# Kernel tuning notes

Measured on AMD Instinct MI355X. Metric: run time of the kernel, lower is better.

The kernel has to match this reference:

```python
import jax, jax.numpy as jnp
import numpy as np

N_NODES = 100000
N_EDGES = 3200000
NFEAT = 256
HDIM = 64
NCLASS = 64
K = 4
ALPHA = 0.1


def setup_inputs() -> dict:
    key = jax.random.key(0)
    k1, k2, k3, k4, k5, k6 = jax.random.split(key, 6)
    x = jax.random.normal(k1, (N_NODES, NFEAT), dtype=jnp.float32)
    edge_index = jax.random.randint(k2, (2, N_EDGES), 0, N_NODES, dtype=jnp.int64)
    W_in = jax.random.normal(k3, (HDIM, NFEAT), dtype=jnp.float32) * (1.0 / np.sqrt(NFEAT))
    b_in = jax.random.normal(k4, (HDIM,), dtype=jnp.float32) * 0.01
    W_out = jax.random.normal(k5, (NCLASS, HDIM), dtype=jnp.float32) * (1.0 / np.sqrt(HDIM))
    b_out = jax.random.normal(k6, (NCLASS,), dtype=jnp.float32) * 0.01
    return {"x": x, "edge_index": edge_index, "W_in": W_in, "b_in": b_in,
            "W_out": W_out, "b_out": b_out}


def _gcn_norm(edge_index, n_nodes):
    # add self-loops, then symmetric normalization (PyG gcn_norm defaults)
    loops = jnp.arange(n_nodes, dtype=edge_index.dtype)
    src = jnp.concatenate([edge_index[0], loops])
    dst = jnp.concatenate([edge_index[1], loops])
    deg = jax.ops.segment_sum(jnp.ones_like(dst, dtype=jnp.float32), dst,
                              num_segments=n_nodes)
    dinv = jnp.where(deg > 0, 1.0 / jnp.sqrt(deg), 0.0)
    w = dinv[src] * dinv[dst]  # [E+N]
    return src, dst, w


def reference(x, edge_index, W_in, b_in, W_out, b_out):
    n = x.shape[0]
    src, dst, w = _gcn_norm(edge_index, n)
    h = x @ W_in.T + b_in                      # [N, 64]
    x0 = h
    for _ in range(K):                         # APPNP: (1-a) * A_hat h + a * x0
        agg = jax.ops.segment_sum(w[:, None] * h[src], dst, num_segments=n)
        h = (1.0 - ALPHA) * agg + ALPHA * x0
    h = jax.nn.relu(h)
    return h @ W_out.T + b_out                 # [N, nclass]
```

## Files before the change

### kernel.cpp

```cpp
#include <hip/hip_runtime.h>
#include <hip/hip_fp16.h>

#define NN 100000
#define NE 3200000
#define NFEAT 256
#define HDIM 64
#define NCLASS 64
#define ALPHA 0.1f
#define CAP 80

#define NB 256
#define BKN 391
#define EBLK (NE / 256)
#define BCAP 24
#define RCAP 96

typedef _Float16 half8 __attribute__((ext_vector_type(8)));
typedef float f32x4 __attribute__((ext_vector_type(4)));


__device__ inline unsigned pack4_fp8(float a, float b, float c, float d) {
    unsigned v = 0;
    v = __builtin_amdgcn_cvt_pk_fp8_f32(a, b, v, false);
    v = __builtin_amdgcn_cvt_pk_fp8_f32(c, d, v, true);
    return v;
}

__device__ inline void acc8_fp8(uint2 r, float m, float* acc) {
    auto l0 = __builtin_amdgcn_cvt_pk_f32_fp8(r.x, false);
    auto h0 = __builtin_amdgcn_cvt_pk_f32_fp8(r.x, true);
    auto l1 = __builtin_amdgcn_cvt_pk_f32_fp8(r.y, false);
    auto h1 = __builtin_amdgcn_cvt_pk_f32_fp8(r.y, true);
    acc[0] = fmaf(m, l0[0], acc[0]); acc[1] = fmaf(m, l0[1], acc[1]);
    acc[2] = fmaf(m, h0[0], acc[2]); acc[3] = fmaf(m, h0[1], acc[3]);
    acc[4] = fmaf(m, l1[0], acc[4]); acc[5] = fmaf(m, l1[1], acc[5]);
    acc[6] = fmaf(m, h1[0], acc[6]); acc[7] = fmaf(m, h1[1], acc[7]);
}


__global__ __launch_bounds__(1024) void bucket_edges(const int* __restrict__ ei,
                                                     unsigned* __restrict__ pairs,
                                                     int* __restrict__ cntg) {
    __shared__ unsigned buf[NB][BCAP];
    __shared__ int cnt[NB];
    __shared__ int rcur[NB];
    int blk = blockIdx.x;
    int t = threadIdx.x;
    int e0 = blk * EBLK;
    for (int i = t; i < NB; i += 1024) { cnt[i] = 0; rcur[i] = 0; }
    __syncthreads();

    for (int eb = 0; eb < EBLK; eb += 1024) {
        bool act = (eb + t) < EBLK;
        if (act) {
            int e = e0 + eb + t;
            unsigned d = (unsigned)ei[NE + e];
            unsigned src = (unsigned)ei[e];
            unsigned b = d / BKN;
            unsigned w = (src << 9) | (d - b * BKN);
            int p = atomicAdd(&cnt[b], 1);
            if (p < BCAP) buf[b][p] = w;
        }
        __syncthreads();
        int lane = t & 63, wv = t >> 6;
        for (int j = 0; j < 16; j++) {
            int b2 = wv * 16 + j;
            int c = cnt[b2]; if (c > BCAP) c = BCAP;
            int rb = rcur[b2];
            if (lane < c) {
                int idx = rb + lane;
                if (idx < RCAP)
                    pairs[((size_t)blk * NB + b2) * RCAP + idx] = buf[b2][lane];
            }
            if (lane == 0) rcur[b2] = rb + c;
        }
        __syncthreads();
        if (t < NB) cnt[t] = 0;
        __syncthreads();
    }
    if (t < NB) cntg[blk * NB + t] = min(rcur[t], RCAP);
}


__global__ __launch_bounds__(1024) void fill_bucket(const unsigned* __restrict__ pairs,
                                                    const int* __restrict__ cntg,
                                                    int* __restrict__ col,
                                                    int* __restrict__ deg,
                                                    float* __restrict__ dinv) {
    __shared__ int cur[BKN];
    __shared__ int pref[NB + 1];
    __shared__ int cnts[NB];
    int b = blockIdx.x;
    int t = threadIdx.x;
    unsigned lo = (unsigned)b * BKN;
    for (int i = t; i < BKN; i += 1024) cur[i] = 0;
    if (t < NB) cnts[t] = cntg[t * NB + b];
    __syncthreads();
    if (t == 0) {
        int run = 0;
        for (int k = 0; k < NB; k++) { pref[k] = run; run += cnts[k]; }
        pref[NB] = run;
    }
    __syncthreads();
    int T = pref[NB];
    for (int i0 = 0; i0 < T; i0 += 1024) {
        int i = i0 + t;
        if (i < T) {
            int l = 0, h = NB;
            while (h - l > 1) { int m = (l + h) >> 1; if (pref[m] <= i) l = m; else h = m; }
            unsigned w = pairs[((size_t)l * NB + b) * RCAP + (i - pref[l])];
            unsigned dl = w & 511;
            unsigned src = w >> 9;
            int slot = atomicAdd(&cur[dl], 1);
            if (slot < CAP && lo + dl < NN)
                col[(size_t)(lo + dl) * CAP + slot] = (int)src;
        }
    }
    __syncthreads();
    for (int i = t; i < BKN; i += 1024) {
        unsigned node = lo + i;
        if (node < NN) {
            int dgv = cur[i];
            deg[node] = dgv;
            dinv[node] = rsqrtf((float)dgv + 1.f);
        }
    }
}


__global__ void prep_w(const float* __restrict__ W, _Float16* __restrict__ W2g,
                       int KG, int Kfull) {
    int i = blockIdx.x * 256 + threadIdx.x;
    if (i >= KG * 64) return;
    int kg = i >> 6;
    int n = i & 63;
    int slot = (kg << 6) + (n ^ ((kg & 3) << 2));
    _Float16 tmp[8];
#pragma unroll
    for (int j = 0; j < 8; j++) tmp[j] = (_Float16)W[n * Kfull + kg * 8 + j];
    *(half8*)&W2g[(size_t)slot * 8] = *(half8*)tmp;
}


__global__ __launch_bounds__(256) void gemm1_mfma(const float* __restrict__ x,
                                                  const _Float16* __restrict__ W2g,
                                                  const float* __restrict__ bias,
                                                  const float* __restrict__ dinv,
                                                  _Float16* __restrict__ g0) {
    __shared__ _Float16 W2[32 * 64 * 8];
    int t = threadIdx.x;
    for (int i = t; i < 2048; i += 256)
        *(half8*)&W2[(size_t)i * 8] = *(const half8*)&W2g[(size_t)i * 8];
    __syncthreads();

    int lane = t & 63;
    int w = t >> 6;
    int r16 = lane & 15, kg = lane >> 4;
    int row0 = blockIdx.x * 128;
    int rowA = row0 + w * 32 + r16;
    int rowB = rowA + 16;
    int rA = rowA < NN ? rowA : NN - 1;
    int rB = rowB < NN ? rowB : NN - 1;
    const float* pa = &x[(size_t)rA * 256 + kg * 8];
    const float* pb = &x[(size_t)rB * 256 + kg * 8];

    f32x4 acc[2][4];
#pragma unroll
    for (int mt = 0; mt < 2; mt++)
#pragma unroll
        for (int nt = 0; nt < 4; nt++) acc[mt][nt] = (f32x4){0.f, 0.f, 0.f, 0.f};

#pragma unroll
    for (int ks = 0; ks < 8; ks++) {
        float4 va0 = *(const float4*)(pa + ks * 32);
        float4 va1 = *(const float4*)(pa + ks * 32 + 4);
        float4 vb0 = *(const float4*)(pb + ks * 32);
        float4 vb1 = *(const float4*)(pb + ks * 32 + 4);
        _Float16 a0h[8] = {(_Float16)va0.x, (_Float16)va0.y, (_Float16)va0.z, (_Float16)va0.w,
                           (_Float16)va1.x, (_Float16)va1.y, (_Float16)va1.z, (_Float16)va1.w};
        _Float16 a1h[8] = {(_Float16)vb0.x, (_Float16)vb0.y, (_Float16)vb0.z, (_Float16)vb0.w,
                           (_Float16)vb1.x, (_Float16)vb1.y, (_Float16)vb1.z, (_Float16)vb1.w};
        half8 a0 = *(half8*)a0h;
        half8 a1 = *(half8*)a1h;
        int kgg = ks * 4 + kg;
#pragma unroll
        for (int nt = 0; nt < 4; nt++) {
            int nidx = nt * 16 + r16;
            int slot = (kgg << 6) + (nidx ^ ((kgg & 3) << 2));
            half8 bfr = *(half8*)&W2[(size_t)slot * 8];
            acc[0][nt] = __builtin_amdgcn_mfma_f32_16x16x32_f16(a0, bfr, acc[0][nt], 0, 0, 0);
            acc[1][nt] = __builtin_amdgcn_mfma_f32_16x16x32_f16(a1, bfr, acc[1][nt], 0, 0, 0);
        }
    }

#pragma unroll
    for (int mt = 0; mt < 2; mt++)
#pragma unroll
        for (int nt = 0; nt < 4; nt++) {
            int colj = nt * 16 + r16;
            float bv = bias[colj];
#pragma unroll
            for (int r = 0; r < 4; r++) {
                int row = row0 + w * 32 + mt * 16 + kg * 4 + r;
                if (row < NN)
                    g0[(size_t)row * 64 + colj] = (_Float16)((acc[mt][nt][r] + bv) * dinv[row]);
            }
        }
}


__global__ __launch_bounds__(256) void cvt_fp16_fp8(const __half* __restrict__ in,
                                                    unsigned char* __restrict__ out) {
    int i = blockIdx.x * 256 + threadIdx.x;
    if (i >= NN * 8) return;
    float4 raw = ((const float4*)in)[i];
    const __half2* h2 = (const __half2*)&raw;
    float f[8];
#pragma unroll
    for (int j = 0; j < 4; j++) {
        float2 v = __half22float2(h2[j]);
        f[2 * j] = v.x; f[2 * j + 1] = v.y;
    }
    uint2 o;
    o.x = pack4_fp8(f[0], f[1], f[2], f[3]);
    o.y = pack4_fp8(f[4], f[5], f[6], f[7]);
    ((uint2*)out)[i] = o;
}


__global__ __launch_bounds__(256) void gemm2_mfma(const float* __restrict__ h,
                                                  const _Float16* __restrict__ W2o,
                                                  const float* __restrict__ bias,
                                                  float* __restrict__ out) {
    __shared__ _Float16 W2[8 * 64 * 8];
    int t = threadIdx.x;
    for (int i = t; i < 512; i += 256)
        *(half8*)&W2[(size_t)i * 8] = *(const half8*)&W2o[(size_t)i * 8];
    __syncthreads();

    int lane = t & 63;
    int w = t >> 6;
    int r16 = lane & 15, kg = lane >> 4;
    int row0 = blockIdx.x * 128;
    int rowA = row0 + w * 32 + r16;
    int rowB = rowA + 16;
    int rA = rowA < NN ? rowA : NN - 1;
    int rB = rowB < NN ? rowB : NN - 1;
    const float* pa = &h[(size_t)rA * 64 + kg * 8];
    const float* pb = &h[(size_t)rB * 64 + kg * 8];

    f32x4 acc[2][4];
#pragma unroll
    for (int mt = 0; mt < 2; mt++)
#pragma unroll
        for (int nt = 0; nt < 4; nt++) acc[mt][nt] = (f32x4){0.f, 0.f, 0.f, 0.f};

#pragma unroll
    for (int ks = 0; ks < 2; ks++) {
        float4 va0 = *(const float4*)(pa + ks * 32);
        float4 va1 = *(const float4*)(pa + ks * 32 + 4);
        float4 vb0 = *(const float4*)(pb + ks * 32);
        float4 vb1 = *(const float4*)(pb + ks * 32 + 4);
        _Float16 a0h[8] = {(_Float16)fmaxf(va0.x, 0.f), (_Float16)fmaxf(va0.y, 0.f),
                           (_Float16)fmaxf(va0.z, 0.f), (_Float16)fmaxf(va0.w, 0.f),
                           (_Float16)fmaxf(va1.x, 0.f), (_Float16)fmaxf(va1.y, 0.f),
                           (_Float16)fmaxf(va1.z, 0.f), (_Float16)fmaxf(va1.w, 0.f)};
        _Float16 a1h[8] = {(_Float16)fmaxf(vb0.x, 0.f), (_Float16)fmaxf(vb0.y, 0.f),
                           (_Float16)fmaxf(vb0.z, 0.f), (_Float16)fmaxf(vb0.w, 0.f),
                           (_Float16)fmaxf(vb1.x, 0.f), (_Float16)fmaxf(vb1.y, 0.f),
                           (_Float16)fmaxf(vb1.z, 0.f), (_Float16)fmaxf(vb1.w, 0.f)};
        half8 a0 = *(half8*)a0h;
        half8 a1 = *(half8*)a1h;
        int kgg = ks * 4 + kg;
#pragma unroll
        for (int nt = 0; nt < 4; nt++) {
            int nidx = nt * 16 + r16;
            int slot = (kgg << 6) + (nidx ^ ((kgg & 3) << 2));
            half8 bfr = *(half8*)&W2[(size_t)slot * 8];
            acc[0][nt] = __builtin_amdgcn_mfma_f32_16x16x32_f16(a0, bfr, acc[0][nt], 0, 0, 0);
            acc[1][nt] = __builtin_amdgcn_mfma_f32_16x16x32_f16(a1, bfr, acc[1][nt], 0, 0, 0);
        }
    }

#pragma unroll
    for (int mt = 0; mt < 2; mt++)
#pragma unroll
        for (int nt = 0; nt < 4; nt++) {
            int colj = nt * 16 + r16;
            float bv = bias[colj];
#pragma unroll
            for (int r = 0; r < 4; r++) {
                int row = row0 + w * 32 + mt * 16 + kg * 4 + r;
                if (row < NN)
                    out[(size_t)row * 64 + colj] = acc[mt][nt][r] + bv;
            }
        }
}


template <bool FINAL>
__global__ __launch_bounds__(256) void appnp_prop_8(const unsigned char* __restrict__ gcur8,
                                                    void* __restrict__ gnext,
                                                    const __half* __restrict__ g0h,
                                                    const float* __restrict__ dinv,
                                                    const int* __restrict__ deg,
                                                    const int* __restrict__ col) {
    int wid = (blockIdx.x * 256 + threadIdx.x) >> 6;
    int lane = threadIdx.x & 63;
    if (wid >= NN) return;
    int eg = lane >> 3;
    int q  = lane & 7;
    const uint2* gc = (const uint2*)gcur8;

    float acc[8];
#pragma unroll
    for (int j = 0; j < 8; j++) acc[j] = 0.f;

    int dg = deg[wid]; if (dg > CAP) dg = CAP;
    int e0 = wid * CAP;
    int end = e0 + dg;
    int p = e0;
    for (; p + 8 < end; p += 16) {
        int i0 = p + eg, i1 = p + 8 + eg;
        float m1 = (i1 < end) ? 1.f : 0.f;
        int s0 = col[i0];
        int s1 = col[(i1 < end) ? i1 : end - 1];
        uint2 r0 = gc[(size_t)s0 * 8 + q];
        uint2 r1 = gc[(size_t)s1 * 8 + q];
        acc8_fp8(r0, 1.f, acc);
        acc8_fp8(r1, m1, acc);
    }
    if (p < end) {
        int i0 = p + eg;
        float m0 = (i0 < end) ? 1.f : 0.f;
        int s0 = col[(i0 < end) ? i0 : end - 1];
        uint2 r0 = gc[(size_t)s0 * 8 + q];
        acc8_fp8(r0, m0, acc);
    }

#pragma unroll
    for (int st = 8; st < 64; st <<= 1) {
#pragma unroll
        for (int j = 0; j < 8; j++) acc[j] += __shfl(acc[j], lane ^ st);
    }

    if (eg == 0) {
        float di = dinv[wid];
        float k = (1.f - ALPHA) * di * di;
        uint2 sraw = gc[(size_t)wid * 8 + q];
        float sf[8];
        {
            auto l0 = __builtin_amdgcn_cvt_pk_f32_fp8(sraw.x, false);
            auto h0 = __builtin_amdgcn_cvt_pk_f32_fp8(sraw.x, true);
            auto l1 = __builtin_amdgcn_cvt_pk_f32_fp8(sraw.y, false);
            auto h1 = __builtin_amdgcn_cvt_pk_f32_fp8(sraw.y, true);
            sf[0] = l0[0]; sf[1] = l0[1]; sf[2] = h0[0]; sf[3] = h0[1];
            sf[4] = l1[0]; sf[5] = l1[1]; sf[6] = h1[0]; sf[7] = h1[1];
        }
        float zf[8];
        {
            float4 zraw = *(const float4*)&g0h[(size_t)wid * 64 + q * 8];
            const __half2* zh = (const __half2*)&zraw;
#pragma unroll
            for (int j = 0; j < 4; j++) {
                float2 v = __half22float2(zh[j]);
                zf[2 * j] = v.x; zf[2 * j + 1] = v.y;
            }
        }
        float g[8];
#pragma unroll
        for (int j = 0; j < 8; j++)
            g[j] = k * (acc[j] + sf[j]) + ALPHA * zf[j];

        if (FINAL) {
            float inv = 1.f / di;
            float* ho = (float*)gnext;
            float4 o0 = make_float4(g[0] * inv, g[1] * inv, g[2] * inv, g[3] * inv);
            float4 o1 = make_float4(g[4] * inv, g[5] * inv, g[6] * inv, g[7] * inv);
            *(float4*)&ho[(size_t)wid * 64 + q * 8]     = o0;
            *(float4*)&ho[(size_t)wid * 64 + q * 8 + 4] = o1;
        } else {
            uint2 o;
            o.x = pack4_fp8(g[0], g[1], g[2], g[3]);
            o.y = pack4_fp8(g[4], g[5], g[6], g[7]);
            ((uint2*)gnext)[(size_t)wid * 8 + q] = o;
        }
    }
}


extern "C" void kernel_launch(void* const* d_in, const int* in_sizes, int n_in,
                              void* d_out, int out_size, void* d_ws, size_t ws_size,
                              hipStream_t stream) {
    const float* x    = (const float*)d_in[0];
    const int*  ei    = (const int*)d_in[1];
    const float* W_in = (const float*)d_in[2];
    const float* b_in = (const float*)d_in[3];
    const float* W_out= (const float*)d_in[4];
    const float* b_out= (const float*)d_in[5];
    float* out = (float*)d_out;

    char* ws = (char*)d_ws;
    size_t off = 0;
    auto alloc = [&](size_t bytes) -> void* {
        void* p = ws + off;
        off = (off + bytes + 255) & ~(size_t)255;
        return p;
    };
    int*      deg  = (int*)    alloc((size_t)NN * 4);
    float*    dinv = (float*)  alloc((size_t)NN * 4);
    int*      cntg = (int*)    alloc((size_t)NB * 256 * 4);
    _Float16* W2g  = (_Float16*)alloc((size_t)32 * 64 * 8 * 2);
    _Float16* W2o  = (_Float16*)alloc((size_t)8 * 64 * 8 * 2);
    int*      col  = (int*)    alloc((size_t)NN * CAP * 4);
    __half*   g0h  = (__half*) alloc((size_t)NN * HDIM * 2);
    unsigned char* g08 = (unsigned char*)alloc((size_t)NN * HDIM);
    unsigned char* gA8 = (unsigned char*)alloc((size_t)NN * HDIM);
    unsigned char* gB8 = (unsigned char*)alloc((size_t)NN * HDIM);
    unsigned* pairs = (unsigned*)g0h;

    bucket_edges<<<256, 1024, 0, stream>>>(ei, pairs, cntg);
    fill_bucket<<<NB, 1024, 0, stream>>>(pairs, cntg, col, deg, dinv);

    prep_w<<<8, 256, 0, stream>>>(W_in, W2g, 32, 256);
    prep_w<<<2, 256, 0, stream>>>(W_out, W2o, 8, 64);

    gemm1_mfma<<<(NN + 127) / 128, 256, 0, stream>>>(x, W2g, b_in, dinv, (_Float16*)g0h);
    cvt_fp16_fp8<<<(NN * 8 + 255) / 256, 256, 0, stream>>>(g0h, g08);

    const int pgrid = (NN * HDIM) / 256;
    appnp_prop_8<false><<<pgrid, 256, 0, stream>>>(g08, gA8, g0h, dinv, deg, col);
    appnp_prop_8<false><<<pgrid, 256, 0, stream>>>(gA8, gB8, g0h, dinv, deg, col);
    appnp_prop_8<false><<<pgrid, 256, 0, stream>>>(gB8, gA8, g0h, dinv, deg, col);
    appnp_prop_8<true ><<<pgrid, 256, 0, stream>>>(gA8, out, g0h, dinv, deg, col);

    gemm2_mfma<<<(NN + 127) / 128, 256, 0, stream>>>(out, W2o, b_out, out);
}
```

Before: 306.3 us.

## Software-pipeline gather loads in APPNP propagation and use packed f32x2 FMAs

Restructures the per-node gather loop in the propagation kernel to process 32 edges per iteration, prefetching the next batch of four neighbor rows before accumulating the current batch. This keeps more independent gather loads in flight per wave. Accumulators become f32x2 vectors so the compiler can emit packed FMA instructions. The cost is extra registers for the double-buffered row data, and more masked wasted loads at the tail for low-degree nodes.

```diff
diff --git a/kernel.cpp b/kernel.cpp
--- a/kernel.cpp
+++ b/kernel.cpp
@@ -17,6 +17,7 @@
 
 typedef _Float16 half8 __attribute__((ext_vector_type(8)));
 typedef float f32x4 __attribute__((ext_vector_type(4)));
+typedef float f32x2 __attribute__((ext_vector_type(2)));
 
 
 __device__ inline unsigned pack4_fp8(float a, float b, float c, float d) {
@@ -26,15 +27,15 @@
     return v;
 }
 
-__device__ inline void acc8_fp8(uint2 r, float m, float* acc) {
-    auto l0 = __builtin_amdgcn_cvt_pk_f32_fp8(r.x, false);
-    auto h0 = __builtin_amdgcn_cvt_pk_f32_fp8(r.x, true);
-    auto l1 = __builtin_amdgcn_cvt_pk_f32_fp8(r.y, false);
-    auto h1 = __builtin_amdgcn_cvt_pk_f32_fp8(r.y, true);
-    acc[0] = fmaf(m, l0[0], acc[0]); acc[1] = fmaf(m, l0[1], acc[1]);
-    acc[2] = fmaf(m, h0[0], acc[2]); acc[3] = fmaf(m, h0[1], acc[3]);
-    acc[4] = fmaf(m, l1[0], acc[4]); acc[5] = fmaf(m, l1[1], acc[5]);
-    acc[6] = fmaf(m, h1[0], acc[6]); acc[7] = fmaf(m, h1[1], acc[7]);
+__device__ inline void acc8_fp8p(uint2 r, f32x2 mm, f32x2* acc2) {
+    f32x2 l0 = __builtin_amdgcn_cvt_pk_f32_fp8(r.x, false);
+    f32x2 h0 = __builtin_amdgcn_cvt_pk_f32_fp8(r.x, true);
+    f32x2 l1 = __builtin_amdgcn_cvt_pk_f32_fp8(r.y, false);
+    f32x2 h1 = __builtin_amdgcn_cvt_pk_f32_fp8(r.y, true);
+    acc2[0] += mm * l0;
+    acc2[1] += mm * h0;
+    acc2[2] += mm * l1;
+    acc2[3] += mm * h1;
 }
 
 
@@ -312,36 +313,53 @@
     int q  = lane & 7;
     const uint2* gc = (const uint2*)gcur8;
 
-    float acc[8];
-#pragma unroll
-    for (int j = 0; j < 8; j++) acc[j] = 0.f;
+    f32x2 acc2[4];
+#pragma unroll
+    for (int j = 0; j < 4; j++) acc2[j] = (f32x2){0.f, 0.f};
 
     int dg = deg[wid]; if (dg > CAP) dg = CAP;
     int e0 = wid * CAP;
     int end = e0 + dg;
-    int p = e0;
-    for (; p + 8 < end; p += 16) {
-        int i0 = p + eg, i1 = p + 8 + eg;
-        float m1 = (i1 < end) ? 1.f : 0.f;
-        int s0 = col[i0];
-        int s1 = col[(i1 < end) ? i1 : end - 1];
-        uint2 r0 = gc[(size_t)s0 * 8 + q];
-        uint2 r1 = gc[(size_t)s1 * 8 + q];
-        acc8_fp8(r0, 1.f, acc);
-        acc8_fp8(r1, m1, acc);
-    }
-    if (p < end) {
-        int i0 = p + eg;
-        float m0 = (i0 < end) ? 1.f : 0.f;
-        int s0 = col[(i0 < end) ? i0 : end - 1];
-        uint2 r0 = gc[(size_t)s0 * 8 + q];
-        acc8_fp8(r0, m0, acc);
+
+    uint2 r[4];
+    f32x2 m[4];
+    if (e0 < end) {
+#pragma unroll
+        for (int j = 0; j < 4; j++) {
+            int i = e0 + j * 8 + eg;
+            float mv = (i < end) ? 1.f : 0.f;
+            int s = col[(i < end) ? i : end - 1];
+            r[j] = gc[(size_t)s * 8 + q];
+            m[j] = (f32x2){mv, mv};
+        }
+        int p = e0;
+        for (; p + 32 < end; p += 32) {
+            uint2 r2[4];
+            f32x2 m2[4];
+#pragma unroll
+            for (int j = 0; j < 4; j++) {
+                int i = p + 32 + j * 8 + eg;
+                float mv = (i < end) ? 1.f : 0.f;
+                int s = col[(i < end) ? i : end - 1];
+                r2[j] = gc[(size_t)s * 8 + q];
+                m2[j] = (f32x2){mv, mv};
+            }
+#pragma unroll
+            for (int j = 0; j < 4; j++) acc8_fp8p(r[j], m[j], acc2);
+#pragma unroll
+            for (int j = 0; j < 4; j++) { r[j] = r2[j]; m[j] = m2[j]; }
+        }
+#pragma unroll
+        for (int j = 0; j < 4; j++) acc8_fp8p(r[j], m[j], acc2);
     }
 
 #pragma unroll
     for (int st = 8; st < 64; st <<= 1) {
 #pragma unroll
-        for (int j = 0; j < 8; j++) acc[j] += __shfl(acc[j], lane ^ st);
+        for (int j = 0; j < 4; j++) {
+            acc2[j][0] += __shfl(acc2[j][0], lane ^ st);
+            acc2[j][1] += __shfl(acc2[j][1], lane ^ st);
+        }
     }
 
     if (eg == 0) {
@@ -370,7 +388,7 @@
         float g[8];
 #pragma unroll
         for (int j = 0; j < 8; j++)
-            g[j] = k * (acc[j] + sf[j]) + ALPHA * zf[j];
+            g[j] = k * (acc2[j >> 1][j & 1] + sf[j]) + ALPHA * zf[j];
 
         if (FINAL) {
             float inv = 1.f / di;
```

Result: faster. 295.3 us (-3.6%).
